# Optimization experiments

Hardware: AMD Instinct MI355X
Metric: run time of the kernel (lower is better)

## Reference

```python
import jax, jax.numpy as jnp
import numpy as np

PATCH = 2      # patch_size
NQ = 4         # n_qubits (state vector has 2**NQ amplitudes)
NL = 2         # n_layers
IMG = 28
NB = IMG // PATCH          # 14 patch blocks per side
NP = NB * NB               # 196 patches


def _bc(c, ndim):
    # broadcast a (B,P) or scalar coefficient against the remaining wire axes
    return c.reshape(c.shape + (1,) * (ndim - c.ndim)) if jnp.ndim(c) else c


def _apply_ry(state, theta, w):
    # state: (B, P, 2,2,2,2); theta: scalar or (B, P)
    st = jnp.moveaxis(state, 2 + w, -1)
    s0, s1 = st[..., 0], st[..., 1]
    h = theta * 0.5
    c = _bc(jnp.cos(h), s0.ndim)
    s = _bc(jnp.sin(h), s0.ndim)
    st = jnp.stack([c * s0 - s * s1, s * s0 + c * s1], axis=-1)
    return jnp.moveaxis(st, -1, 2 + w)


def _apply_rz(state, theta, w):
    st = jnp.moveaxis(state, 2 + w, -1)
    ph = _bc(jnp.exp(-0.5j * theta), st[..., 0].ndim)  # e^{-i theta/2}
    st = jnp.stack([ph * st[..., 0], jnp.conj(ph) * st[..., 1]], axis=-1)
    return jnp.moveaxis(st, -1, 2 + w)


def _apply_cnot(state, cw, tw):
    # control wire cw, target wire tw (cw < tw)
    st = jnp.moveaxis(state, (2 + cw, 2 + tw), (-2, -1))
    c0 = st[..., 0, :]
    c1 = jnp.stack([st[..., 1, 1], st[..., 1, 0]], axis=-1)  # flip target when control=1
    st = jnp.stack([c0, c1], axis=-2)
    return jnp.moveaxis(st, (-2, -1), (2 + cw, 2 + tw))


def _simulate(angles, var_params):
    # angles: (B, NP, NQ) encoder RY angles (pixel values); var_params: (NL, 2, NQ)
    B, P, _ = angles.shape
    state = jnp.zeros((B, P, 2 ** NQ), jnp.complex64).at[:, :, 0].set(1.0)
    state = state.reshape((B, P) + (2,) * NQ)
    for w in range(NQ):                       # GeneralEncoder: RY(x_i) on wire i
        state = _apply_ry(state, angles[:, :, w], w)
    for l in range(NL):                       # variational layers
        for w in range(NQ):
            state = _apply_ry(state, var_params[l, 0, w], w)
        for w in range(NQ):
            state = _apply_rz(state, var_params[l, 1, w], w)
        for c in range(NQ - 1):               # CNOT entanglement chain
            state = _apply_cnot(state, c, c + 1)
    probs = state.real ** 2 + state.imag ** 2  # (B, P, 2,2,2,2)
    exps = []
    for w in range(NQ):                        # <Z_w> = P(bit_w=0) - P(bit_w=1)
        other = tuple(2 + k for k in range(NQ) if k != w)
        p = probs.sum(axis=other)              # (B, P, 2)
        exps.append(p[..., 0] - p[..., 1])
    return jnp.stack(exps, axis=-1)            # (B, P, NQ)


def setup_inputs() -> dict:
    key = jax.random.key(0)
    k1, k2, k3 = jax.random.split(key, 3)
    B = 2048
    x = jax.random.uniform(k1, (B, IMG, IMG), dtype=jnp.float32)
    var_params = jax.random.normal(k2, (NL, 2, NQ), dtype=jnp.float32)
    W = jax.random.normal(k3, (10, NP * NQ), dtype=jnp.float32) * 0.03
    b = jnp.zeros((10,), dtype=jnp.float32)
    return {"x": x, "var_params": var_params, "W": W, "b": b}


def reference(x, var_params, W, b):
    B = x.shape[0]
    # extract non-overlapping PATCHxPATCH patches, row-major within patch
    patches = x.reshape(B, NB, PATCH, NB, PATCH).transpose(0, 1, 3, 2, 4)
    patches = patches.reshape(B, NP, PATCH * PATCH)
    meas = _simulate(patches, var_params)      # (B, NP, NQ)
    feats = meas.reshape(B, NP * NQ)           # patch-major concat, matches torch.cat
    logits = feats @ W.T + b
    return jax.nn.log_softmax(logits, axis=-1)
```

## Files before the change

### kernel.cpp

```cpp
#include <hip/hip_runtime.h>
#include <math.h>

#define NPATCH 196
#define NFEAT  784
#define NCLS   10


template<int STRIDE>
__device__ __forceinline__ void ry_gate(float* sr, float* si, float c, float s) {
    #pragma unroll
    for (int g = 0; g < 8; ++g) {
        const int lo = g & (STRIDE - 1);
        const int s0 = ((g ^ lo) << 1) | lo;
        const int s1 = s0 | STRIDE;
        float r0 = sr[s0], r1 = sr[s1];
        float i0 = si[s0], i1 = si[s1];
        sr[s0] = c * r0 - s * r1;  sr[s1] = s * r0 + c * r1;
        si[s0] = c * i0 - s * i1;  si[s1] = s * i0 + c * i1;
    }
}

template<int STRIDE>
__device__ __forceinline__ void rz_gate(float* sr, float* si, float c, float s) {
    #pragma unroll
    for (int idx = 0; idx < 16; ++idx) {
        float r = sr[idx], im = si[idx];
        if (idx & STRIDE) { sr[idx] = c * r - s * im; si[idx] = c * im + s * r; }
        else              { sr[idx] = c * r + s * im; si[idx] = c * im - s * r; }
    }
}

template<int SC, int ST>
__device__ __forceinline__ void cnot_gate(float* sr, float* si) {
    #pragma unroll
    for (int idx = 0; idx < 16; ++idx) {
        if ((idx & SC) && !(idx & ST)) {
            const int j = idx | ST;
            float tr = sr[idx]; sr[idx] = sr[j]; sr[j] = tr;
            float ti = si[idx]; si[idx] = si[j]; si[j] = ti;
        }
    }
}

__global__ __launch_bounds__(256)
void quanv_fused(const float* __restrict__ x, const float* __restrict__ vp,
                 const float* __restrict__ W, const float* __restrict__ bias,
                 float* __restrict__ out) {
    __shared__ float feats[NFEAT];
    __shared__ float redbuf[4][NCLS];
    __shared__ float logitsS[NCLS];

    const int b = blockIdx.x;
    const int t = threadIdx.x;

    if (t < NPATCH) {
        const int i = t / 14;
        const int j = t - i * 14;
        const float* xb = x + b * 784;
        const float* r0p = xb + (2 * i) * 28 + 2 * j;
        const float* r1p = r0p + 28;
        const float a0 = r0p[0], a1 = r0p[1], a2 = r1p[0], a3 = r1p[1];

        float ec[4], es[4];
        __sincosf(0.5f * a0, &es[0], &ec[0]);
        __sincosf(0.5f * a1, &es[1], &ec[1]);
        __sincosf(0.5f * a2, &es[2], &ec[2]);
        __sincosf(0.5f * a3, &es[3], &ec[3]);

        float sr[16], si[16];
        #pragma unroll
        for (int s = 0; s < 16; ++s) {
            const float v = ((s & 8) ? es[0] : ec[0]) * ((s & 4) ? es[1] : ec[1])
                          * ((s & 2) ? es[2] : ec[2]) * ((s & 1) ? es[3] : ec[3]);
            sr[s] = v;
            si[s] = 0.0f;
        }

        #pragma unroll
        for (int l = 0; l < 2; ++l) {
            const float* p = vp + l * 8;
            float gc, gs;
            __sincosf(0.5f * p[0], &gs, &gc); ry_gate<8>(sr, si, gc, gs);
            __sincosf(0.5f * p[1], &gs, &gc); ry_gate<4>(sr, si, gc, gs);
            __sincosf(0.5f * p[2], &gs, &gc); ry_gate<2>(sr, si, gc, gs);
            __sincosf(0.5f * p[3], &gs, &gc); ry_gate<1>(sr, si, gc, gs);
            __sincosf(0.5f * p[4], &gs, &gc); rz_gate<8>(sr, si, gc, gs);
            __sincosf(0.5f * p[5], &gs, &gc); rz_gate<4>(sr, si, gc, gs);
            __sincosf(0.5f * p[6], &gs, &gc); rz_gate<2>(sr, si, gc, gs);
            __sincosf(0.5f * p[7], &gs, &gc); rz_gate<1>(sr, si, gc, gs);
            cnot_gate<8, 4>(sr, si);
            cnot_gate<4, 2>(sr, si);
            cnot_gate<2, 1>(sr, si);
        }

        float e0 = 0.f, e1 = 0.f, e2 = 0.f, e3 = 0.f;
        #pragma unroll
        for (int s = 0; s < 16; ++s) {
            const float pr = sr[s] * sr[s] + si[s] * si[s];
            e0 += (s & 8) ? -pr : pr;
            e1 += (s & 4) ? -pr : pr;
            e2 += (s & 2) ? -pr : pr;
            e3 += (s & 1) ? -pr : pr;
        }
        feats[t * 4 + 0] = e0;
        feats[t * 4 + 1] = e1;
        feats[t * 4 + 2] = e2;
        feats[t * 4 + 3] = e3;
    }
    __syncthreads();

    float acc[NCLS];
    #pragma unroll
    for (int c = 0; c < NCLS; ++c) acc[c] = 0.0f;
    for (int k = t; k < NFEAT; k += 256) {
        const float f = feats[k];
        #pragma unroll
        for (int c = 0; c < NCLS; ++c) acc[c] += f * W[c * NFEAT + k];
    }
    #pragma unroll
    for (int off = 32; off > 0; off >>= 1) {
        #pragma unroll
        for (int c = 0; c < NCLS; ++c) acc[c] += __shfl_down(acc[c], off, 64);
    }
    const int wave = t >> 6, lane = t & 63;
    if (lane == 0) {
        #pragma unroll
        for (int c = 0; c < NCLS; ++c) redbuf[wave][c] = acc[c];
    }
    __syncthreads();
    if (t < NCLS) {
        logitsS[t] = redbuf[0][t] + redbuf[1][t] + redbuf[2][t] + redbuf[3][t] + bias[t];
    }
    __syncthreads();
    if (t < NCLS) {
        float m = -1e30f;
        #pragma unroll
        for (int c = 0; c < NCLS; ++c) m = fmaxf(m, logitsS[c]);
        float ssum = 0.0f;
        #pragma unroll
        for (int c = 0; c < NCLS; ++c) ssum += __expf(logitsS[c] - m);
        out[b * NCLS + t] = logitsS[t] - m - __logf(ssum);
    }
}

extern "C" void kernel_launch(void* const* d_in, const int* in_sizes, int n_in,
                              void* d_out, int out_size, void* d_ws, size_t ws_size,
                              hipStream_t stream) {
    const float* x  = (const float*)d_in[0];
    const float* vp = (const float*)d_in[1];
    const float* W  = (const float*)d_in[2];
    const float* bb = (const float*)d_in[3];
    float* out = (float*)d_out;

    quanv_fused<<<2048, 256, 0, stream>>>(x, vp, W, bb, out);
}
```

Baseline: 81.44 us.

## Precompute gate tables, merge RZ phases, exploit real state, fuse readout into GEMV

Gate cosines and sines, plus the combined per-basis-state phase of the four RZ gates in each layer, are computed once per block into shared memory instead of being evaluated per thread. The first layer runs on a real-valued state, so its RY gates skip the imaginary parts, and each layer's four RZ gates become a single diagonal phase multiply. Each patch thread now multiplies its four expectations directly with float4 rows of W, which removes the shared-memory feature buffer and one barrier. An extra barrier is added for the tables, and the expectation sums are computed with a butterfly tree.

Result: faster. 73.24 us (-10.1%).

```diff
diff --git a/kernel.cpp b/kernel.cpp
--- a/kernel.cpp
+++ b/kernel.cpp
@@ -2,12 +2,24 @@
 #include <math.h>
 
 #define NPATCH 196
-#define NFEAT  784
 #define NCLS   10
 
 
 template<int STRIDE>
-__device__ __forceinline__ void ry_gate(float* sr, float* si, float c, float s) {
+__device__ __forceinline__ void ry_real(float* sr, float c, float s) {
+    #pragma unroll
+    for (int g = 0; g < 8; ++g) {
+        const int lo = g & (STRIDE - 1);
+        const int s0 = ((g ^ lo) << 1) | lo;
+        const int s1 = s0 | STRIDE;
+        float r0 = sr[s0], r1 = sr[s1];
+        sr[s0] = c * r0 - s * r1;
+        sr[s1] = s * r0 + c * r1;
+    }
+}
+
+template<int STRIDE>
+__device__ __forceinline__ void ry_cplx(float* sr, float* si, float c, float s) {
     #pragma unroll
     for (int g = 0; g < 8; ++g) {
         const int lo = g & (STRIDE - 1);
@@ -17,16 +29,6 @@
         float i0 = si[s0], i1 = si[s1];
         sr[s0] = c * r0 - s * r1;  sr[s1] = s * r0 + c * r1;
         si[s0] = c * i0 - s * i1;  si[s1] = s * i0 + c * i1;
-    }
-}
-
-template<int STRIDE>
-__device__ __forceinline__ void rz_gate(float* sr, float* si, float c, float s) {
-    #pragma unroll
-    for (int idx = 0; idx < 16; ++idx) {
-        float r = sr[idx], im = si[idx];
-        if (idx & STRIDE) { sr[idx] = c * r - s * im; si[idx] = c * im + s * r; }
-        else              { sr[idx] = c * r + s * im; si[idx] = c * im - s * r; }
     }
 }
 
@@ -46,12 +48,37 @@
 void quanv_fused(const float* __restrict__ x, const float* __restrict__ vp,
                  const float* __restrict__ W, const float* __restrict__ bias,
                  float* __restrict__ out) {
-    __shared__ float feats[NFEAT];
+    __shared__ float ry_t[2][4][2];
+    __shared__ float ph_t[2][16][2];
     __shared__ float redbuf[4][NCLS];
     __shared__ float logitsS[NCLS];
 
     const int b = blockIdx.x;
     const int t = threadIdx.x;
+
+    if (t < 40) {
+        float vc, vs;
+        if (t < 32) {
+            const int l = t >> 4, k = t & 15;
+            const float* rz = vp + l * 8 + 4;
+            float phi = ((k >> 3) & 1) ? 0.5f * rz[0] : -0.5f * rz[0];
+            phi      += ((k >> 2) & 1) ? 0.5f * rz[1] : -0.5f * rz[1];
+            phi      += ((k >> 1) & 1) ? 0.5f * rz[2] : -0.5f * rz[2];
+            phi      += ( k       & 1) ? 0.5f * rz[3] : -0.5f * rz[3];
+            __sincosf(phi, &vs, &vc);
+            ph_t[l][k][0] = vc; ph_t[l][k][1] = vs;
+        } else {
+            const int idx = t - 32, l = idx >> 2, w = idx & 3;
+            float h = 0.5f * vp[l * 8 + w];
+            __sincosf(h, &vs, &vc);
+            ry_t[l][w][0] = vc; ry_t[l][w][1] = vs;
+        }
+    }
+    __syncthreads();
+
+    float acc[NCLS];
+    #pragma unroll
+    for (int c = 0; c < NCLS; ++c) acc[c] = 0.0f;
 
     if (t < NPATCH) {
         const int i = t / 14;
@@ -67,56 +94,64 @@
         __sincosf(0.5f * a2, &es[2], &ec[2]);
         __sincosf(0.5f * a3, &es[3], &ec[3]);
 
+        float p01[4], p23[4];
+        p01[0] = ec[0] * ec[1]; p01[1] = ec[0] * es[1];
+        p01[2] = es[0] * ec[1]; p01[3] = es[0] * es[1];
+        p23[0] = ec[2] * ec[3]; p23[1] = ec[2] * es[3];
+        p23[2] = es[2] * ec[3]; p23[3] = es[2] * es[3];
         float sr[16], si[16];
         #pragma unroll
-        for (int s = 0; s < 16; ++s) {
-            const float v = ((s & 8) ? es[0] : ec[0]) * ((s & 4) ? es[1] : ec[1])
-                          * ((s & 2) ? es[2] : ec[2]) * ((s & 1) ? es[3] : ec[3]);
-            sr[s] = v;
-            si[s] = 0.0f;
+        for (int s = 0; s < 16; ++s) sr[s] = p01[s >> 2] * p23[s & 3];
+
+        ry_real<8>(sr, ry_t[0][0][0], ry_t[0][0][1]);
+        ry_real<4>(sr, ry_t[0][1][0], ry_t[0][1][1]);
+        ry_real<2>(sr, ry_t[0][2][0], ry_t[0][2][1]);
+        ry_real<1>(sr, ry_t[0][3][0], ry_t[0][3][1]);
+        #pragma unroll
+        for (int k = 0; k < 16; ++k) {
+            float r = sr[k];
+            sr[k] = r * ph_t[0][k][0];
+            si[k] = r * ph_t[0][k][1];
         }
+        cnot_gate<8, 4>(sr, si);
+        cnot_gate<4, 2>(sr, si);
+        cnot_gate<2, 1>(sr, si);
 
+        ry_cplx<8>(sr, si, ry_t[1][0][0], ry_t[1][0][1]);
+        ry_cplx<4>(sr, si, ry_t[1][1][0], ry_t[1][1][1]);
+        ry_cplx<2>(sr, si, ry_t[1][2][0], ry_t[1][2][1]);
+        ry_cplx<1>(sr, si, ry_t[1][3][0], ry_t[1][3][1]);
         #pragma unroll
-        for (int l = 0; l < 2; ++l) {
-            const float* p = vp + l * 8;
-            float gc, gs;
-            __sincosf(0.5f * p[0], &gs, &gc); ry_gate<8>(sr, si, gc, gs);
-            __sincosf(0.5f * p[1], &gs, &gc); ry_gate<4>(sr, si, gc, gs);
-            __sincosf(0.5f * p[2], &gs, &gc); ry_gate<2>(sr, si, gc, gs);
-            __sincosf(0.5f * p[3], &gs, &gc); ry_gate<1>(sr, si, gc, gs);
-            __sincosf(0.5f * p[4], &gs, &gc); rz_gate<8>(sr, si, gc, gs);
-            __sincosf(0.5f * p[5], &gs, &gc); rz_gate<4>(sr, si, gc, gs);
-            __sincosf(0.5f * p[6], &gs, &gc); rz_gate<2>(sr, si, gc, gs);
-            __sincosf(0.5f * p[7], &gs, &gc); rz_gate<1>(sr, si, gc, gs);
-            cnot_gate<8, 4>(sr, si);
-            cnot_gate<4, 2>(sr, si);
-            cnot_gate<2, 1>(sr, si);
+        for (int k = 0; k < 16; ++k) {
+            float c = ph_t[1][k][0], s = ph_t[1][k][1];
+            float r = sr[k], im = si[k];
+            sr[k] = r * c - im * s;
+            si[k] = im * c + r * s;
         }
+        cnot_gate<8, 4>(sr, si);
+        cnot_gate<4, 2>(sr, si);
+        cnot_gate<2, 1>(sr, si);
 
-        float e0 = 0.f, e1 = 0.f, e2 = 0.f, e3 = 0.f;
+        float p[16];
         #pragma unroll
-        for (int s = 0; s < 16; ++s) {
-            const float pr = sr[s] * sr[s] + si[s] * si[s];
-            e0 += (s & 8) ? -pr : pr;
-            e1 += (s & 4) ? -pr : pr;
-            e2 += (s & 2) ? -pr : pr;
-            e3 += (s & 1) ? -pr : pr;
+        for (int k = 0; k < 16; ++k) p[k] = sr[k] * sr[k] + si[k] * si[k];
+        float q[8], e3 = 0.f;
+        #pragma unroll
+        for (int k = 0; k < 8; ++k) { e3 += p[2*k] - p[2*k+1]; q[k] = p[2*k] + p[2*k+1]; }
+        float r4[4], e2 = 0.f;
+        #pragma unroll
+        for (int k = 0; k < 4; ++k) { e2 += q[2*k] - q[2*k+1]; r4[k] = q[2*k] + q[2*k+1]; }
+        const float e1 = (r4[0] - r4[1]) + (r4[2] - r4[3]);
+        const float e0 = (r4[0] + r4[1]) - (r4[2] + r4[3]);
+
+        const float4* __restrict__ W4 = (const float4*)W;
+        #pragma unroll
+        for (int c = 0; c < NCLS; ++c) {
+            const float4 w = W4[c * 196 + t];
+            acc[c] = e0 * w.x + e1 * w.y + e2 * w.z + e3 * w.w;
         }
-        feats[t * 4 + 0] = e0;
-        feats[t * 4 + 1] = e1;
-        feats[t * 4 + 2] = e2;
-        feats[t * 4 + 3] = e3;
     }
-    __syncthreads();
 
-    float acc[NCLS];
-    #pragma unroll
-    for (int c = 0; c < NCLS; ++c) acc[c] = 0.0f;
-    for (int k = t; k < NFEAT; k += 256) {
-        const float f = feats[k];
-        #pragma unroll
-        for (int c = 0; c < NCLS; ++c) acc[c] += f * W[c * NFEAT + k];
-    }
     #pragma unroll
     for (int off = 32; off > 0; off >>= 1) {
         #pragma unroll
```

## Fold gates algebraically and restructure the linear head with vectorized loads

Applied to the files above, without the earlier changes.

Merges the first variational RY layer into the encoder angles and builds the product state from factored pair products. The layer-1 RZ gates become one precomputed diagonal phase table, so the state only turns complex once. Later gates are pruned: the layer-2 RZ layer is dropped since it is diagonal and does not change the Z-basis measurement, and the final CNOT chain is skipped. The final CNOT chain is a permutation before the Z measurement, so dropping it is only valid if the expectation formula is rewritten to match, and that rewritten formula should be checked for correctness. The linear layer now uses float4 feature and weight loads with 16-lane groups per class, replacing the 10-accumulator reduction across the block.

Result: faster. 71.20 us (-12.6%).

```diff
diff --git a/kernel.cpp b/kernel.cpp
--- a/kernel.cpp
+++ b/kernel.cpp
@@ -1,13 +1,11 @@
 #include <hip/hip_runtime.h>
 #include <math.h>
 
-#define NPATCH 196
-#define NFEAT  784
-#define NCLS   10
+#define NCLS 10
 
 
 template<int STRIDE>
-__device__ __forceinline__ void ry_gate(float* sr, float* si, float c, float s) {
+__device__ __forceinline__ void ry_cplx(float* sr, float* si, float c, float s) {
     #pragma unroll
     for (int g = 0; g < 8; ++g) {
         const int lo = g & (STRIDE - 1);
@@ -17,16 +15,6 @@
         float i0 = si[s0], i1 = si[s1];
         sr[s0] = c * r0 - s * r1;  sr[s1] = s * r0 + c * r1;
         si[s0] = c * i0 - s * i1;  si[s1] = s * i0 + c * i1;
-    }
-}
-
-template<int STRIDE>
-__device__ __forceinline__ void rz_gate(float* sr, float* si, float c, float s) {
-    #pragma unroll
-    for (int idx = 0; idx < 16; ++idx) {
-        float r = sr[idx], im = si[idx];
-        if (idx & STRIDE) { sr[idx] = c * r - s * im; si[idx] = c * im + s * r; }
-        else              { sr[idx] = c * r + s * im; si[idx] = c * im - s * r; }
     }
 }
 
@@ -46,99 +34,123 @@
 void quanv_fused(const float* __restrict__ x, const float* __restrict__ vp,
                  const float* __restrict__ W, const float* __restrict__ bias,
                  float* __restrict__ out) {
-    __shared__ float feats[NFEAT];
-    __shared__ float redbuf[4][NCLS];
+    __shared__ float ph_c[16], ph_s[16];
+    __shared__ float ry1c[4], ry1s[4];
+    __shared__ float4 feats4[196];
     __shared__ float logitsS[NCLS];
 
     const int b = blockIdx.x;
     const int t = threadIdx.x;
 
-    if (t < NPATCH) {
+    if (t >= 224 && t < 244) {
+        const int u = t - 224;
+        float vc, vs;
+        if (u < 16) {
+            const float* rz = vp + 4;
+            float phi = ((u & 8) ? 0.5f : -0.5f) * rz[0]
+                      + ((u & 4) ? 0.5f : -0.5f) * rz[1]
+                      + ((u & 2) ? 0.5f : -0.5f) * rz[2]
+                      + ((u & 1) ? 0.5f : -0.5f) * rz[3];
+            __sincosf(phi, &vs, &vc);
+            ph_c[u] = vc; ph_s[u] = vs;
+        } else {
+            const int w = u - 16;
+            __sincosf(0.5f * vp[8 + w], &vs, &vc);
+            ry1c[w] = vc; ry1s[w] = vs;
+        }
+    }
+
+    const bool is_sim = (t < 196);
+    float sr[16];
+    if (is_sim) {
         const int i = t / 14;
         const int j = t - i * 14;
-        const float* xb = x + b * 784;
-        const float* r0p = xb + (2 * i) * 28 + 2 * j;
-        const float* r1p = r0p + 28;
-        const float a0 = r0p[0], a1 = r0p[1], a2 = r1p[0], a3 = r1p[1];
+        const float* xb = x + b * 784 + 2 * i * 28 + 2 * j;
+        const float2 A  = *(const float2*)xb;
+        const float2 Bv = *(const float2*)(xb + 28);
 
         float ec[4], es[4];
-        __sincosf(0.5f * a0, &es[0], &ec[0]);
-        __sincosf(0.5f * a1, &es[1], &ec[1]);
-        __sincosf(0.5f * a2, &es[2], &ec[2]);
-        __sincosf(0.5f * a3, &es[3], &ec[3]);
+        __sincosf(0.5f * (A.x  + vp[0]), &es[0], &ec[0]);
+        __sincosf(0.5f * (A.y  + vp[1]), &es[1], &ec[1]);
+        __sincosf(0.5f * (Bv.x + vp[2]), &es[2], &ec[2]);
+        __sincosf(0.5f * (Bv.y + vp[3]), &es[3], &ec[3]);
 
-        float sr[16], si[16];
+        float p01[4], p23[4];
+        p01[0] = ec[0] * ec[1]; p01[1] = ec[0] * es[1];
+        p01[2] = es[0] * ec[1]; p01[3] = es[0] * es[1];
+        p23[0] = ec[2] * ec[3]; p23[1] = ec[2] * es[3];
+        p23[2] = es[2] * ec[3]; p23[3] = es[2] * es[3];
         #pragma unroll
-        for (int s = 0; s < 16; ++s) {
-            const float v = ((s & 8) ? es[0] : ec[0]) * ((s & 4) ? es[1] : ec[1])
-                          * ((s & 2) ? es[2] : ec[2]) * ((s & 1) ? es[3] : ec[3]);
-            sr[s] = v;
-            si[s] = 0.0f;
-        }
-
-        #pragma unroll
-        for (int l = 0; l < 2; ++l) {
-            const float* p = vp + l * 8;
-            float gc, gs;
-            __sincosf(0.5f * p[0], &gs, &gc); ry_gate<8>(sr, si, gc, gs);
-            __sincosf(0.5f * p[1], &gs, &gc); ry_gate<4>(sr, si, gc, gs);
-            __sincosf(0.5f * p[2], &gs, &gc); ry_gate<2>(sr, si, gc, gs);
-            __sincosf(0.5f * p[3], &gs, &gc); ry_gate<1>(sr, si, gc, gs);
-            __sincosf(0.5f * p[4], &gs, &gc); rz_gate<8>(sr, si, gc, gs);
-            __sincosf(0.5f * p[5], &gs, &gc); rz_gate<4>(sr, si, gc, gs);
-            __sincosf(0.5f * p[6], &gs, &gc); rz_gate<2>(sr, si, gc, gs);
-            __sincosf(0.5f * p[7], &gs, &gc); rz_gate<1>(sr, si, gc, gs);
-            cnot_gate<8, 4>(sr, si);
-            cnot_gate<4, 2>(sr, si);
-            cnot_gate<2, 1>(sr, si);
-        }
-
-        float e0 = 0.f, e1 = 0.f, e2 = 0.f, e3 = 0.f;
-        #pragma unroll
-        for (int s = 0; s < 16; ++s) {
-            const float pr = sr[s] * sr[s] + si[s] * si[s];
-            e0 += (s & 8) ? -pr : pr;
-            e1 += (s & 4) ? -pr : pr;
-            e2 += (s & 2) ? -pr : pr;
-            e3 += (s & 1) ? -pr : pr;
-        }
-        feats[t * 4 + 0] = e0;
-        feats[t * 4 + 1] = e1;
-        feats[t * 4 + 2] = e2;
-        feats[t * 4 + 3] = e3;
+        for (int s = 0; s < 16; ++s) sr[s] = p01[s >> 2] * p23[s & 3];
     }
     __syncthreads();
 
-    float acc[NCLS];
-    #pragma unroll
-    for (int c = 0; c < NCLS; ++c) acc[c] = 0.0f;
-    for (int k = t; k < NFEAT; k += 256) {
-        const float f = feats[k];
+    if (is_sim) {
+        float si_[16];
         #pragma unroll
-        for (int c = 0; c < NCLS; ++c) acc[c] += f * W[c * NFEAT + k];
-    }
-    #pragma unroll
-    for (int off = 32; off > 0; off >>= 1) {
+        for (int k = 0; k < 16; ++k) {
+            float r = sr[k];
+            sr[k]  = r * ph_c[k];
+            si_[k] = r * ph_s[k];
+        }
+        cnot_gate<8, 4>(sr, si_);
+        cnot_gate<4, 2>(sr, si_);
+        cnot_gate<2, 1>(sr, si_);
+
+        ry_cplx<8>(sr, si_, ry1c[0], ry1s[0]);
+        ry_cplx<4>(sr, si_, ry1c[1], ry1s[1]);
+        ry_cplx<2>(sr, si_, ry1c[2], ry1s[2]);
+        ry_cplx<1>(sr, si_, ry1c[3], ry1s[3]);
+
+        float p[16];
         #pragma unroll
-        for (int c = 0; c < NCLS; ++c) acc[c] += __shfl_down(acc[c], off, 64);
-    }
-    const int wave = t >> 6, lane = t & 63;
-    if (lane == 0) {
+        for (int k = 0; k < 16; ++k) p[k] = sr[k] * sr[k] + si_[k] * si_[k];
+
+        float s8[8], d8[8];
         #pragma unroll
-        for (int c = 0; c < NCLS; ++c) redbuf[wave][c] = acc[c];
+        for (int k = 0; k < 8; ++k) { s8[k] = p[2*k] + p[2*k+1]; d8[k] = p[2*k] - p[2*k+1]; }
+        const float e3 =  d8[0] - d8[1] - d8[2] + d8[3] - d8[4] + d8[5] + d8[6] - d8[7];
+        const float e2 =  s8[0] - s8[1] - s8[2] + s8[3] - s8[4] + s8[5] + s8[6] - s8[7];
+        float S0 = s8[0] + s8[1], S1 = s8[2] + s8[3], S2 = s8[4] + s8[5], S3 = s8[6] + s8[7];
+        const float e1 = S0 - S1 - S2 + S3;
+        const float e0 = S0 + S1 - S2 - S3;
+
+        feats4[t] = make_float4(e0, e1, e2, e3);
     }
     __syncthreads();
-    if (t < NCLS) {
-        logitsS[t] = redbuf[0][t] + redbuf[1][t] + redbuf[2][t] + redbuf[3][t] + bias[t];
+
+    const int c = t >> 4, j = t & 15;
+    float acc = 0.0f;
+    if (c < NCLS) {
+        const float4* __restrict__ W4 = (const float4*)W;
+        #pragma unroll
+        for (int i2 = 0; i2 < 12; ++i2) {
+            const int v = j + 16 * i2;
+            const float4 f = feats4[v];
+            const float4 w = W4[c * 196 + v];
+            acc += f.x * w.x + f.y * w.y + f.z * w.z + f.w * w.w;
+        }
+        if (j < 4) {
+            const int v = j + 192;
+            const float4 f = feats4[v];
+            const float4 w = W4[c * 196 + v];
+            acc += f.x * w.x + f.y * w.y + f.z * w.z + f.w * w.w;
+        }
     }
+    acc += __shfl_down(acc, 8, 16);
+    acc += __shfl_down(acc, 4, 16);
+    acc += __shfl_down(acc, 2, 16);
+    acc += __shfl_down(acc, 1, 16);
+    if (j == 0 && c < NCLS) logitsS[c] = acc + bias[c];
     __syncthreads();
+
     if (t < NCLS) {
         float m = -1e30f;
         #pragma unroll
-        for (int c = 0; c < NCLS; ++c) m = fmaxf(m, logitsS[c]);
+        for (int k = 0; k < NCLS; ++k) m = fmaxf(m, logitsS[k]);
         float ssum = 0.0f;
         #pragma unroll
-        for (int c = 0; c < NCLS; ++c) ssum += __expf(logitsS[c] - m);
+        for (int k = 0; k < NCLS; ++k) ssum += __expf(logitsS[k] - m);
         out[b * NCLS + t] = logitsS[t] - m - __logf(ssum);
     }
 }
```
